# Kernel tuning notes

Measured on AMD Instinct MI355X. Metric: run time of the kernel, lower is better.

Reference implementation:

```python
import jax, jax.numpy as jnp
import numpy as np

B, C, H, W = 512, 1, 64, 64
T, L, Z = 32, 1024, 128
RS, WS = 12, 12


def _filterbank(g_x, g_y, logvar, logdelta, N):
    # g_x, g_y, logvar, logdelta: (B, 1)
    g_x = 0.5 * (W + 1) * (g_x + 1)
    g_y = 0.5 * (H + 1) * (g_y + 1)
    delta = (max(H, W) - 1) / (N - 1) * jnp.exp(logdelta)            # (B,1)
    offs = jnp.arange(1.0, 1.0 + N) - 0.5 * (N + 1)                  # (N,)
    mu_x = g_x + offs * delta                                        # (B,N)
    mu_y = g_y + offs * delta                                        # (B,N)
    inv2var = 0.5 / jnp.exp(logvar)[:, :, None]                      # (B,1,1)
    Fx = jnp.exp(-inv2var * (jnp.arange(1.0, 1.0 + W)[None, None, :] - mu_x[:, :, None]) ** 2)
    Fx = Fx / jnp.sum(Fx + 1e-8, axis=2, keepdims=True)              # (B,N,W)
    Fy = jnp.exp(-inv2var * (jnp.arange(1.0, 1.0 + H)[None, None, :] - mu_y[:, :, None]) ** 2)
    Fy = Fy / jnp.sum(Fy + 1e-8, axis=2, keepdims=True)              # (B,N,H)
    return Fx, Fy


def _lstm(x, h, c, Wih, Whh, bih, bhh):
    g = x @ Wih.T + bih + h @ Whh.T + bhh
    i, f, gg, o = jnp.split(g, 4, axis=1)
    c = jax.nn.sigmoid(f) * c + jax.nn.sigmoid(i) * jnp.tanh(gg)
    h = jax.nn.sigmoid(o) * jnp.tanh(c)
    return h, c


def setup_inputs() -> dict:
    key = jax.random.key(0)
    ks = jax.random.split(key, 9)
    s = 0.02
    return {
        'x': jax.random.uniform(ks[0], (B, C * H * W), jnp.float32),
        'enc_Wih': jax.random.normal(ks[1], (4 * L, 2 * RS * RS + L), jnp.float32) * s,
        'enc_Whh': jax.random.normal(ks[2], (4 * L, L), jnp.float32) * s,
        'enc_bih': jnp.zeros((4 * L,), jnp.float32),
        'enc_bhh': jnp.zeros((4 * L,), jnp.float32),
        'dec_Wih': jax.random.normal(ks[3], (4 * L, Z), jnp.float32) * s,
        'dec_Whh': jax.random.normal(ks[4], (4 * L, L), jnp.float32) * s,
        'dec_bih': jnp.zeros((4 * L,), jnp.float32),
        'dec_bhh': jnp.zeros((4 * L,), jnp.float32),
        'zW': jax.random.normal(ks[5], (2 * Z, L), jnp.float32) * s,
        'zb': jnp.zeros((2 * Z,), jnp.float32),
        'wW': jax.random.normal(ks[6], (WS * WS, L), jnp.float32) * s,
        'wb': jnp.zeros((WS * WS,), jnp.float32),
        'raW': jax.random.normal(ks[7], (5, L), jnp.float32) * s,
        'rab': jnp.zeros((5,), jnp.float32),
        'waW': jax.random.normal(ks[8], (5, L), jnp.float32) * s,
        'wab': jnp.zeros((5,), jnp.float32),
    }


def reference(x, enc_Wih, enc_Whh, enc_bih, enc_bhh, dec_Wih, dec_Whh, dec_bih, dec_bhh,
              zW, zb, wW, wb, raW, rab, waW, wab):
    def read(xf, x_hat, h_dec):
        a = h_dec @ raW.T + rab                                      # (B,5)
        g_x, g_y, logvar, logdelta, loggamma = jnp.split(a, 5, axis=1)
        Fx, Fy = _filterbank(g_x, g_y, logvar, logdelta, RS)
        nx = jnp.einsum('bnh,bhw,bmw->bnm', Fy, xf.reshape(-1, H, W), Fx)
        nxh = jnp.einsum('bnh,bhw,bmw->bnm', Fy, x_hat.reshape(-1, H, W), Fx)
        return jnp.exp(loggamma) * jnp.concatenate(
            [nx.reshape(nx.shape[0], -1), nxh.reshape(nxh.shape[0], -1)], axis=1)

    def write(h_dec):
        w = h_dec @ wW.T + wb                                        # (B, WS*WS)
        a = h_dec @ waW.T + wab
        g_x, g_y, logvar, logdelta, loggamma = jnp.split(a, 5, axis=1)
        Fx, Fy = _filterbank(g_x, g_y, logvar, logdelta, WS)
        wr = jnp.einsum('bnh,bnm,bmw->bhw', Fy, w.reshape(-1, WS, WS), Fx)
        return jnp.exp(-loggamma) * wr.reshape(wr.shape[0], -1)

    zkeys = jax.random.split(jax.random.key(42), T)

    def step(carry, key):
        c, h_enc, c_enc, h_dec, c_dec = carry
        x_hat = x - jax.nn.sigmoid(c)
        r = read(x, x_hat, h_dec)
        h_enc, c_enc = _lstm(jnp.concatenate([r, h_dec], axis=1), h_enc, c_enc,
                             enc_Wih, enc_Whh, enc_bih, enc_bhh)
        stats = h_enc @ zW.T + zb
        mu, logsig = jnp.split(stats, 2, axis=1)
        sig = jnp.exp(logsig)
        z = mu + sig * jax.random.normal(key, mu.shape, mu.dtype)
        h_dec, c_dec = _lstm(z, h_dec, c_dec, dec_Wih, dec_Whh, dec_bih, dec_bhh)
        c = c + write(h_dec)
        return (c, h_enc, c_enc, h_dec, c_dec), (mu, sig)

    c0 = jnp.zeros_like(x)
    h0 = jnp.zeros((x.shape[0], L), x.dtype)
    carry0 = (c0, h0, h0, h0, h0)
    (c, _, _, _, _), (mus, sigs) = jax.lax.scan(step, carry0, zkeys)
    # stack along last dim like torch.stack(mus, dim=-1): (B, Z, T)
    return c, jnp.moveaxis(mus, 0, -1), jnp.moveaxis(sigs, 0, -1)
```

## Files before the change

kernel.cpp:

```cpp
#include <hip/hip_runtime.h>
#include <cstdint>
#include <cstddef>

#define BB 512
#define TT 32
#define LL 1024
#define ZZ 128

typedef unsigned short ushort_t;
typedef __attribute__((ext_vector_type(8))) short s8v;
typedef __attribute__((ext_vector_type(4))) float f32x4;

__device__ __forceinline__ float sigf(float x) { return 1.0f / (1.0f + expf(-x)); }

__device__ __forceinline__ ushort_t f2bf(float f) {
  uint32_t u = __float_as_uint(f);
  uint32_t r = (u + 0x7FFFu + ((u >> 16) & 1u)) >> 16;
  return (ushort_t)r;
}
__device__ __forceinline__ float bf2f(ushort_t h) {
  return __uint_as_float(((uint32_t)h) << 16);
}
__device__ __forceinline__ void splitf(float v, ushort_t& hi, ushort_t& lo) {
  hi = f2bf(v);
  lo = f2bf(v - bf2f(hi));
}

__device__ __forceinline__ float jax_erfinv(float x) {
  float w = -log1pf(-x * x);
  float p;
  if (w < 5.0f) {
    w = w - 2.5f;
    p = 2.81022636e-08f;
    p = fmaf(p, w, 3.43273939e-07f);
    p = fmaf(p, w, -3.5233877e-06f);
    p = fmaf(p, w, -4.39150654e-06f);
    p = fmaf(p, w, 0.00021858087f);
    p = fmaf(p, w, -0.00125372503f);
    p = fmaf(p, w, -0.00417768164f);
    p = fmaf(p, w, 0.246640727f);
    p = fmaf(p, w, 1.50140941f);
  } else {
    w = sqrtf(w) - 3.0f;
    p = -0.000200214257f;
    p = fmaf(p, w, 0.000100950558f);
    p = fmaf(p, w, 0.00134934322f);
    p = fmaf(p, w, -0.00367342844f);
    p = fmaf(p, w, 0.00573950773f);
    p = fmaf(p, w, -0.0076224613f);
    p = fmaf(p, w, 0.00943887047f);
    p = fmaf(p, w, 1.00167406f);
    p = fmaf(p, w, 2.83297682f);
  }
  return p * x;
}

__device__ __forceinline__ void threefry(uint32_t k0, uint32_t k1,
                                         uint32_t x0, uint32_t x1,
                                         uint32_t& o0, uint32_t& o1) {
  uint32_t ks0 = k0, ks1 = k1, ks2 = k0 ^ k1 ^ 0x1BD11BDAu;
  x0 += ks0; x1 += ks1;
#define TF_ROT(x, d) (((x) << (d)) | ((x) >> (32 - (d))))
#define TF_RND(r) { x0 += x1; x1 = TF_ROT(x1, r); x1 ^= x0; }
  TF_RND(13) TF_RND(15) TF_RND(26) TF_RND(6)
  x0 += ks1; x1 += ks2 + 1u;
  TF_RND(17) TF_RND(29) TF_RND(16) TF_RND(24)
  x0 += ks2; x1 += ks0 + 2u;
  TF_RND(13) TF_RND(15) TF_RND(26) TF_RND(6)
  x0 += ks0; x1 += ks1 + 3u;
  TF_RND(17) TF_RND(29) TF_RND(16) TF_RND(24)
  x0 += ks1; x1 += ks2 + 4u;
  TF_RND(13) TF_RND(15) TF_RND(26) TF_RND(6)
  x0 += ks2; x1 += ks0 + 5u;
#undef TF_RND
#undef TF_ROT
  o0 = x0; o1 = x1;
}

__device__ __forceinline__ float bits_to_normal(uint32_t bits) {
  uint32_t fb = (bits >> 9) | 0x3f800000u;
  float f = __uint_as_float(fb) - 1.0f;
  const float lo = -0.99999994f;
  float u = fmaxf(lo, f * 2.0f + lo);
  return 1.41421356237f * jax_erfinv(u);
}

__global__ __launch_bounds__(256) void k_split(const float* __restrict__ src,
                                               ushort_t* __restrict__ hi,
                                               ushort_t* __restrict__ lo, int n) {
  int i = blockIdx.x * 256 + threadIdx.x;
  if (i >= n) return;
  ushort_t h, l;
  splitf(src[i], h, l);
  hi[i] = h; lo[i] = l;
}

__global__ void k_catbias(const float* __restrict__ wb, const float* __restrict__ wab,
                          float* __restrict__ cb) {
  int i = threadIdx.x;
  cb[i] = (i < 144) ? wb[i] : (i < 149 ? wab[i - 144] : 0.f);
}

struct Seg { const ushort_t* A; const ushort_t* W; int K; int lda; int ldw; };
struct SegList { Seg s[9]; int n; };

__device__ __forceinline__ void load_tiles(const Seg& sg, int bm, int bn, int N, int k0,
                                           int tid, s8v va[4], s8v vw[4]) {
#pragma unroll
  for (int i = 0; i < 4; ++i) {
    int cch = tid + 256 * i;
    int row = cch >> 3, col = cch & 7;
    va[i] = *(const s8v*)(sg.A + (size_t)(bm + row) * sg.lda + k0 + col * 8);
    int n = bn + row;
    if (n < N) vw[i] = *(const s8v*)(sg.W + (size_t)n * sg.ldw + k0 + col * 8);
    else       vw[i] = (s8v)(short)0;
  }
}

__global__ __launch_bounds__(256, 2) void mfma_gemm(
    float* __restrict__ C, unsigned zstride, int N, SegList segs, int ipz, int T) {
  __shared__ __align__(16) ushort_t As[128][72];
  __shared__ __align__(16) ushort_t Ws[128][72];
  const int z = blockIdx.z;
  C += (size_t)z * zstride;
  const int bm = blockIdx.y * 128, bn = blockIdx.x * 128;
  const int tid = threadIdx.x;
  const int w = tid >> 6, lane = tid & 63;
  const int wr = w >> 1, wc = w & 1;
  const int lr = lane & 15, lq = lane >> 4;
  f32x4 acc[4][4] = {};

  int it0 = z * ipz;
  int it1 = it0 + ipz; if (it1 > T) it1 = T;
  int iters = it1 - it0;
  if (iters > 0) {
    int si = 0, rem = it0;
    while (rem >= (segs.s[si].K >> 6)) { rem -= segs.s[si].K >> 6; ++si; }
    int k0 = rem << 6;
    s8v va[4], vw[4];
    load_tiles(segs.s[si], bm, bn, N, k0, tid, va, vw);
    for (int it = 0; it < iters; ++it) {
      __syncthreads();
#pragma unroll
      for (int i = 0; i < 4; ++i) {
        int cch = tid + 256 * i;
        *(s8v*)&As[cch >> 3][(cch & 7) * 8] = va[i];
        *(s8v*)&Ws[cch >> 3][(cch & 7) * 8] = vw[i];
      }
      __syncthreads();
      int nsi = si, nk0 = k0 + 64;
      if (nk0 >= segs.s[si].K) { nk0 = 0; ++nsi; }
      if (it + 1 < iters) load_tiles(segs.s[nsi], bm, bn, N, nk0, tid, va, vw);
#pragma unroll
      for (int ks = 0; ks < 2; ++ks) {
        s8v af[4], bf[4];
#pragma unroll
        for (int m = 0; m < 4; ++m)
          af[m] = *(const s8v*)&As[wr * 64 + m * 16 + lr][ks * 32 + lq * 8];
#pragma unroll
        for (int j = 0; j < 4; ++j)
          bf[j] = *(const s8v*)&Ws[wc * 64 + j * 16 + lr][ks * 32 + lq * 8];
#pragma unroll
        for (int m = 0; m < 4; ++m)
#pragma unroll
          for (int j = 0; j < 4; ++j)
            acc[m][j] = __builtin_amdgcn_mfma_f32_16x16x32_bf16(af[m], bf[j], acc[m][j], 0, 0, 0);
      }
      si = nsi; k0 = nk0;
    }
  }
#pragma unroll
  for (int j = 0; j < 4; ++j) {
    int col = bn + wc * 64 + j * 16 + lr;
    if (col < N) {
#pragma unroll
      for (int m = 0; m < 4; ++m)
#pragma unroll
        for (int q = 0; q < 4; ++q) {
          int rr = bm + wr * 64 + m * 16 + lq * 4 + q;
          C[(size_t)rr * N + col] = acc[m][j][q];
        }
    }
  }
}

__global__ __launch_bounds__(256) void k_fread(
    const float* __restrict__ x, const float* __restrict__ c,
    const float* __restrict__ rab,
    ushort_t* __restrict__ rH, ushort_t* __restrict__ rL) {
  int b = blockIdx.x;
  __shared__ float a_sh[5];
  __shared__ float fx[12][64], fy[12][64];
  __shared__ float srow[24];
  __shared__ float X[64][64];
  __shared__ float Xh[64][64];
  __shared__ float tmp[12][64], tmph[12][64];
  int tid = threadIdx.x;
  if (tid < 5) a_sh[tid] = rab[tid];
  for (int e = tid; e < 4096; e += 256) {
    float xv = x[(size_t)b * 4096 + e];
    float cv = c[(size_t)b * 4096 + e];
    X[e >> 6][e & 63] = xv;
    Xh[e >> 6][e & 63] = xv - sigf(cv);
  }
  __syncthreads();
  float gx = 32.5f * (a_sh[0] + 1.f);
  float gy = 32.5f * (a_sh[1] + 1.f);
  float i2v = 0.5f * expf(-a_sh[2]);
  float delta = (63.f / 11.f) * expf(a_sh[3]);
  float gam = expf(a_sh[4]);
  for (int e = tid; e < 768; e += 256) {
    int n = e >> 6, p = e & 63;
    float mu_x = gx + ((float)n - 5.5f) * delta;
    float mu_y = gy + ((float)n - 5.5f) * delta;
    float dx = (float)(p + 1) - mu_x;
    float dy = (float)(p + 1) - mu_y;
    fx[n][p] = expf(-i2v * dx * dx);
    fy[n][p] = expf(-i2v * dy * dy);
  }
  __syncthreads();
  if (tid < 24) {
    int n = tid % 12;
    float s = 0.f;
    if (tid < 12) { for (int p = 0; p < 64; ++p) s += fx[n][p]; }
    else          { for (int p = 0; p < 64; ++p) s += fy[n][p]; }
    srow[tid] = s + 6.4e-7f;
  }
  __syncthreads();
  for (int e = tid; e < 768; e += 256) {
    int n = e >> 6, p = e & 63;
    fx[n][p] /= srow[n];
    fy[n][p] /= srow[12 + n];
  }
  __syncthreads();
  for (int e = tid; e < 768; e += 256) {
    int n = e >> 6, w2 = e & 63;
    float s = 0.f, sh = 0.f;
    for (int hh = 0; hh < 64; ++hh) {
      float f = fy[n][hh];
      s  = fmaf(f, X[hh][w2], s);
      sh = fmaf(f, Xh[hh][w2], sh);
    }
    tmp[n][w2] = s; tmph[n][w2] = sh;
  }
  __syncthreads();
  if (tid < 144) {
    int n = tid / 12, m = tid % 12;
    float s = 0.f, sh = 0.f;
    for (int w2 = 0; w2 < 64; ++w2) {
      float f = fx[m][w2];
      s  = fmaf(tmp[n][w2], f, s);
      sh = fmaf(tmph[n][w2], f, sh);
    }
    float v0 = gam * s, v1 = gam * sh;
    size_t i0 = (size_t)b * 320 + n * 12 + m;
    size_t i1 = i0 + 144;
    ushort_t h0, l0, h1, l1;
    splitf(v0, h0, l0); splitf(v1, h1, l1);
    rH[i0] = h0; rL[i0] = l0;
    rH[i1] = h1; rL[i1] = l1;
  }
}

__global__ __launch_bounds__(256) void k_z(const float* __restrict__ parts,
                                           unsigned SZ, int nz,
                                           const float* __restrict__ zb,
                                           ushort_t* __restrict__ zH,
                                           ushort_t* __restrict__ zL,
                                           float* __restrict__ out_mu,
                                           float* __restrict__ out_sg, int t) {
  int i = blockIdx.x * 256 + threadIdx.x;
  int b = i >> 7, zi = i & 127;
  float mu = zb[zi], ls = zb[128 + zi];
  for (int z = 0; z < nz; ++z) {
    size_t base = (size_t)z * SZ + (size_t)b * 256;
    mu += parts[base + zi];
    ls += parts[base + 128 + zi];
  }
  uint32_t kA, kB, o0, o1;
  threefry(0u, 42u, 0u, (uint32_t)t, kA, kB);
  threefry(kA, kB, 0u, (uint32_t)i, o0, o1);
  float ep = bits_to_normal(o0 ^ o1);
  float sg = expf(ls);
  float zv = mu + sg * ep;
  ushort_t zh, zl;
  splitf(zv, zh, zl);
  zH[i] = zh; zL[i] = zl;
  out_mu[(size_t)b * 4096 + zi * 32 + t] = mu;
  out_sg[(size_t)b * 4096 + zi * 32 + t] = sg;
}

__global__ __launch_bounds__(256) void k_fwr(
    float* __restrict__ c, const float* __restrict__ x,
    const float* __restrict__ parts, unsigned WZ, int nz,
    const float* __restrict__ cb, const float* __restrict__ rab,
    ushort_t* __restrict__ rH, ushort_t* __restrict__ rL, int last) {
  int b = blockIdx.x;
  __shared__ float red[160];
  __shared__ float a_sh[5];
  __shared__ float fx[12][64], fy[12][64];
  __shared__ float srow[24];
  __shared__ float tmp[12][64], tmph[12][64];
  __shared__ float X[64][64];
  __shared__ float Xh[64][64];
  int tid = threadIdx.x;
  if (tid < 154) {
    float s = cb[tid];
    for (int z = 0; z < nz; ++z) s += parts[(size_t)z * WZ + (size_t)b * 176 + tid];
    red[tid] = s;
  }
  __syncthreads();
  {
    float gx = 32.5f * (red[144] + 1.f);
    float gy = 32.5f * (red[145] + 1.f);
    float i2v = 0.5f * expf(-red[146]);
    float delta = (63.f / 11.f) * expf(red[147]);
    for (int e = tid; e < 768; e += 256) {
      int n = e >> 6, p = e & 63;
      float mu_x = gx + ((float)n - 5.5f) * delta;
      float mu_y = gy + ((float)n - 5.5f) * delta;
      float dx = (float)(p + 1) - mu_x;
      float dy = (float)(p + 1) - mu_y;
      fx[n][p] = expf(-i2v * dx * dx);
      fy[n][p] = expf(-i2v * dy * dy);
    }
  }
  __syncthreads();
  if (tid < 24) {
    int n = tid % 12;
    float s = 0.f;
    if (tid < 12) { for (int p = 0; p < 64; ++p) s += fx[n][p]; }
    else          { for (int p = 0; p < 64; ++p) s += fy[n][p]; }
    srow[tid] = s + 6.4e-7f;
  }
  __syncthreads();
  for (int e = tid; e < 768; e += 256) {
    int n = e >> 6, p = e & 63;
    fx[n][p] /= srow[n];
    fy[n][p] /= srow[12 + n];
  }
  __syncthreads();
  for (int e = tid; e < 768; e += 256) {
    int n = e >> 6, w2 = e & 63;
    float s = 0.f;
#pragma unroll
    for (int m = 0; m < 12; ++m) s = fmaf(red[n * 12 + m], fx[m][w2], s);
    tmp[n][w2] = s;
  }
  __syncthreads();
  {
    float gam = expf(-red[148]);
    for (int e = tid; e < 4096; e += 256) {
      int hh = e >> 6, w2 = e & 63;
      float s = 0.f;
#pragma unroll
      for (int n = 0; n < 12; ++n) s = fmaf(fy[n][hh], tmp[n][w2], s);
      float cv = c[(size_t)b * 4096 + e] + gam * s;
      c[(size_t)b * 4096 + e] = cv;
      float xv = x[(size_t)b * 4096 + e];
      X[hh][w2] = xv;
      Xh[hh][w2] = xv - sigf(cv);
    }
  }
  if (last) return;
  if (tid < 5) a_sh[tid] = red[149 + tid] + rab[tid];
  __syncthreads();
  {
    float gx = 32.5f * (a_sh[0] + 1.f);
    float gy = 32.5f * (a_sh[1] + 1.f);
    float i2v = 0.5f * expf(-a_sh[2]);
    float delta = (63.f / 11.f) * expf(a_sh[3]);
    for (int e = tid; e < 768; e += 256) {
      int n = e >> 6, p = e & 63;
      float mu_x = gx + ((float)n - 5.5f) * delta;
      float mu_y = gy + ((float)n - 5.5f) * delta;
      float dx = (float)(p + 1) - mu_x;
      float dy = (float)(p + 1) - mu_y;
      fx[n][p] = expf(-i2v * dx * dx);
      fy[n][p] = expf(-i2v * dy * dy);
    }
  }
  __syncthreads();
  if (tid < 24) {
    int n = tid % 12;
    float s = 0.f;
    if (tid < 12) { for (int p = 0; p < 64; ++p) s += fx[n][p]; }
    else          { for (int p = 0; p < 64; ++p) s += fy[n][p]; }
    srow[tid] = s + 6.4e-7f;
  }
  __syncthreads();
  for (int e = tid; e < 768; e += 256) {
    int n = e >> 6, p = e & 63;
    fx[n][p] /= srow[n];
    fy[n][p] /= srow[12 + n];
  }
  __syncthreads();
  for (int e = tid; e < 768; e += 256) {
    int n = e >> 6, w2 = e & 63;
    float s = 0.f, sh = 0.f;
    for (int hh = 0; hh < 64; ++hh) {
      float f = fy[n][hh];
      s  = fmaf(f, X[hh][w2], s);
      sh = fmaf(f, Xh[hh][w2], sh);
    }
    tmp[n][w2] = s; tmph[n][w2] = sh;
  }
  __syncthreads();
  if (tid < 144) {
    float gam = expf(a_sh[4]);
    int n = tid / 12, m = tid % 12;
    float s = 0.f, sh = 0.f;
    for (int w2 = 0; w2 < 64; ++w2) {
      float f = fx[m][w2];
      s  = fmaf(tmp[n][w2], f, s);
      sh = fmaf(tmph[n][w2], f, sh);
    }
    float v0 = gam * s, v1 = gam * sh;
    size_t i0 = (size_t)b * 320 + n * 12 + m;
    size_t i1 = i0 + 144;
    ushort_t h0, l0, h1, l1;
    splitf(v0, h0, l0); splitf(v1, h1, l1);
    rH[i0] = h0; rL[i0] = l0;
    rH[i1] = h1; rL[i1] = l1;
  }
}

typedef unsigned short us4 __attribute__((ext_vector_type(4)));
__global__ __launch_bounds__(256) void k_lstm(const float* __restrict__ g,
                                              unsigned GZ, int nz,
                                              const float* __restrict__ bih,
                                              const float* __restrict__ bhh,
                                              float* __restrict__ cst,
                                              ushort_t* __restrict__ hH,
                                              ushort_t* __restrict__ hL) {
  int q = blockIdx.x * 256 + threadIdx.x;
  int b = q >> 8, uq = q & 255;
  size_t base = (size_t)b * 1024;
  float4 ig = *(const float4*)&bih[uq * 4];
  float4 fg = *(const float4*)&bih[1024 + uq * 4];
  float4 gg = *(const float4*)&bih[2048 + uq * 4];
  float4 og = *(const float4*)&bih[3072 + uq * 4];
  {
    float4 t0 = *(const float4*)&bhh[uq * 4];
    float4 t1 = *(const float4*)&bhh[1024 + uq * 4];
    float4 t2 = *(const float4*)&bhh[2048 + uq * 4];
    float4 t3 = *(const float4*)&bhh[3072 + uq * 4];
    ig.x += t0.x; ig.y += t0.y; ig.z += t0.z; ig.w += t0.w;
    fg.x += t1.x; fg.y += t1.y; fg.z += t1.z; fg.w += t1.w;
    gg.x += t2.x; gg.y += t2.y; gg.z += t2.z; gg.w += t2.w;
    og.x += t3.x; og.y += t3.y; og.z += t3.z; og.w += t3.w;
  }
  for (int z = 0; z < nz; ++z) {
    const float* gz = g + (size_t)z * GZ + base * 4;
    float4 t0 = *(const float4*)&gz[uq * 4];
    float4 t1 = *(const float4*)&gz[1024 + uq * 4];
    float4 t2 = *(const float4*)&gz[2048 + uq * 4];
    float4 t3 = *(const float4*)&gz[3072 + uq * 4];
    ig.x += t0.x; ig.y += t0.y; ig.z += t0.z; ig.w += t0.w;
    fg.x += t1.x; fg.y += t1.y; fg.z += t1.z; fg.w += t1.w;
    gg.x += t2.x; gg.y += t2.y; gg.z += t2.z; gg.w += t2.w;
    og.x += t3.x; og.y += t3.y; og.z += t3.z; og.w += t3.w;
  }
  float4 cv = *(const float4*)&cst[(size_t)q * 4];
  float cva[4] = {cv.x, cv.y, cv.z, cv.w};
  float iga[4] = {ig.x, ig.y, ig.z, ig.w};
  float fga[4] = {fg.x, fg.y, fg.z, fg.w};
  float gga[4] = {gg.x, gg.y, gg.z, gg.w};
  float oga[4] = {og.x, og.y, og.z, og.w};
  us4 hhv, hlv;
  float cvo[4];
#pragma unroll
  for (int j = 0; j < 4; ++j) {
    float cnew = sigf(fga[j]) * cva[j] + sigf(iga[j]) * tanhf(gga[j]);
    cvo[j] = cnew;
    float hv = sigf(oga[j]) * tanhf(cnew);
    ushort_t hh, hl;
    splitf(hv, hh, hl);
    hhv[j] = hh; hlv[j] = hl;
  }
  *(float4*)&cst[(size_t)q * 4] = make_float4(cvo[0], cvo[1], cvo[2], cvo[3]);
  *(us4*)&hH[(size_t)q * 4] = hhv;
  *(us4*)&hL[(size_t)q * 4] = hlv;
}

extern "C" void kernel_launch(void* const* d_in, const int* in_sizes, int n_in,
                              void* d_out, int out_size, void* d_ws, size_t ws_size,
                              hipStream_t stream) {
  const float* x       = (const float*)d_in[0];
  const float* enc_Wih = (const float*)d_in[1];
  const float* enc_Whh = (const float*)d_in[2];
  const float* enc_bih = (const float*)d_in[3];
  const float* enc_bhh = (const float*)d_in[4];
  const float* dec_Wih = (const float*)d_in[5];
  const float* dec_Whh = (const float*)d_in[6];
  const float* dec_bih = (const float*)d_in[7];
  const float* dec_bhh = (const float*)d_in[8];
  const float* zW  = (const float*)d_in[9];
  const float* zb  = (const float*)d_in[10];
  const float* wW  = (const float*)d_in[11];
  const float* wb  = (const float*)d_in[12];
  const float* raW = (const float*)d_in[13];
  const float* rab = (const float*)d_in[14];
  const float* waW = (const float*)d_in[15];
  const float* wab = (const float*)d_in[16];

  float* out = (float*)d_out;
  float* c      = out;
  float* out_mu = out + 2097152;
  float* out_sg = out + 4194304;

  int NZ = 4;
  size_t need = 0;
  for (int pass = 0; pass < 2; ++pass) {
    size_t off = 0;
    auto sz = [&](size_t bytes) { off = (off + bytes + 255) & ~(size_t)255; };
    sz(2097152); sz(2097152);
    sz(1048576); sz(1048576); sz(1048576); sz(1048576);
    sz(327680); sz(327680);
    sz(360448); sz(360448);
    sz(131072); sz(131072);
    sz((size_t)NZ * 8388608);
    sz(704);
    sz(10747904); sz(10747904);
    sz(8388608); sz(8388608);
    sz(1048576); sz(1048576);
    sz(8388608); sz(8388608);
    sz(524288); sz(524288);
    need = off;
    if (pass == 0 && ws_size < need) NZ = 2; else break;
  }

  char* base = (char*)d_ws;
  size_t off = 0;
  auto alloc = [&](size_t bytes) -> char* {
    char* p = base + off;
    off = (off + bytes + 255) & ~(size_t)255;
    return p;
  };
  float* c_enc = (float*)alloc(2097152);
  float* c_dec = (float*)alloc(2097152);
  ushort_t* hdH = (ushort_t*)alloc(1048576);
  ushort_t* hdL = (ushort_t*)alloc(1048576);
  ushort_t* heH = (ushort_t*)alloc(1048576);
  ushort_t* heL = (ushort_t*)alloc(1048576);
  ushort_t* rH  = (ushort_t*)alloc(327680);
  ushort_t* rL  = (ushort_t*)alloc(327680);
  ushort_t* cWH = (ushort_t*)alloc(360448);
  ushort_t* cWL = (ushort_t*)alloc(360448);
  size_t zero_bytes = off;
  ushort_t* zH = (ushort_t*)alloc(131072);
  ushort_t* zL = (ushort_t*)alloc(131072);
  float* gbuf  = (float*)alloc((size_t)NZ * 8388608);
  float* cb    = (float*)alloc(704);
  ushort_t* eWihH = (ushort_t*)alloc(10747904);
  ushort_t* eWihL = (ushort_t*)alloc(10747904);
  ushort_t* eWhhH = (ushort_t*)alloc(8388608);
  ushort_t* eWhhL = (ushort_t*)alloc(8388608);
  ushort_t* dWihH = (ushort_t*)alloc(1048576);
  ushort_t* dWihL = (ushort_t*)alloc(1048576);
  ushort_t* dWhhH = (ushort_t*)alloc(8388608);
  ushort_t* dWhhL = (ushort_t*)alloc(8388608);
  ushort_t* zWH   = (ushort_t*)alloc(524288);
  ushort_t* zWL   = (ushort_t*)alloc(524288);

  hipMemsetAsync(c, 0, (size_t)2097152 * sizeof(float), stream);
  hipMemsetAsync(base, 0, zero_bytes, stream);

  k_split<<<(5373952 + 255) / 256, 256, 0, stream>>>(enc_Wih, eWihH, eWihL, 5373952);
  k_split<<<(4194304 + 255) / 256, 256, 0, stream>>>(enc_Whh, eWhhH, eWhhL, 4194304);
  k_split<<<(524288 + 255) / 256, 256, 0, stream>>>(dec_Wih, dWihH, dWihL, 524288);
  k_split<<<(4194304 + 255) / 256, 256, 0, stream>>>(dec_Whh, dWhhH, dWhhL, 4194304);
  k_split<<<(262144 + 255) / 256, 256, 0, stream>>>(zW, zWH, zWL, 262144);
  k_split<<<(147456 + 255) / 256, 256, 0, stream>>>(wW, cWH, cWL, 147456);
  k_split<<<(5120 + 255) / 256, 256, 0, stream>>>(waW, cWH + 147456, cWL + 147456, 5120);
  k_split<<<(5120 + 255) / 256, 256, 0, stream>>>(raW, cWH + 152576, cWL + 152576, 5120);
  k_catbias<<<1, 176, 0, stream>>>(wb, wab, cb);

  SegList encS;
  encS.n = 9;
  encS.s[0] = {rH,  eWihH,       320,  320, 1312};
  encS.s[1] = {rL,  eWihH,       320,  320, 1312};
  encS.s[2] = {rH,  eWihL,       320,  320, 1312};
  encS.s[3] = {hdH, eWihH + 288, 1024, 1024, 1312};
  encS.s[4] = {hdL, eWihH + 288, 1024, 1024, 1312};
  encS.s[5] = {hdH, eWihL + 288, 1024, 1024, 1312};
  encS.s[6] = {heH, eWhhH,       1024, 1024, 1024};
  encS.s[7] = {heL, eWhhH,       1024, 1024, 1024};
  encS.s[8] = {heH, eWhhL,       1024, 1024, 1024};
  SegList decS;
  decS.n = 6;
  decS.s[0] = {zH,  dWihH, 128,  128, 128};
  decS.s[1] = {zL,  dWihH, 128,  128, 128};
  decS.s[2] = {zH,  dWihL, 128,  128, 128};
  decS.s[3] = {hdH, dWhhH, 1024, 1024, 1024};
  decS.s[4] = {hdL, dWhhH, 1024, 1024, 1024};
  decS.s[5] = {hdH, dWhhL, 1024, 1024, 1024};
  SegList staS;
  staS.n = 3;
  staS.s[0] = {heH, zWH, 1024, 1024, 1024};
  staS.s[1] = {heL, zWH, 1024, 1024, 1024};
  staS.s[2] = {heH, zWL, 1024, 1024, 1024};
  SegList wvS;
  wvS.n = 3;
  wvS.s[0] = {hdH, cWH, 1024, 1024, 1024};
  wvS.s[1] = {hdL, cWH, 1024, 1024, 1024};
  wvS.s[2] = {hdH, cWL, 1024, 1024, 1024};

  const unsigned GZ = 2097152;
  const unsigned SZ = 131072;
  const unsigned WZ = 90112;
  const int ipz_e = (111 + NZ - 1) / NZ;
  const int ipz_d = (54 + NZ - 1) / NZ;

  k_fread<<<512, 256, 0, stream>>>(x, c, rab, rH, rL);
  for (int t = 0; t < TT; ++t) {
    mfma_gemm<<<dim3(32, 4, NZ), 256, 0, stream>>>(gbuf, GZ, 4096, encS, ipz_e, 111);
    k_lstm<<<512, 256, 0, stream>>>(gbuf, GZ, NZ, enc_bih, enc_bhh, c_enc, heH, heL);
    mfma_gemm<<<dim3(2, 4, 8), 256, 0, stream>>>(gbuf, SZ, 256, staS, 6, 48);
    k_z<<<256, 256, 0, stream>>>(gbuf, SZ, 8, zb, zH, zL, out_mu, out_sg, t);
    mfma_gemm<<<dim3(32, 4, NZ), 256, 0, stream>>>(gbuf, GZ, 4096, decS, ipz_d, 54);
    k_lstm<<<512, 256, 0, stream>>>(gbuf, GZ, NZ, dec_bih, dec_bhh, c_dec, hdH, hdL);
    mfma_gemm<<<dim3(2, 4, 8), 256, 0, stream>>>(gbuf, WZ, 176, wvS, 6, 48);
    k_fwr<<<512, 256, 0, stream>>>(c, x, gbuf, WZ, 8, cb, rab, rH, rL, t == TT - 1);
  }
}
```

Measured before the change: 3.918 ms.

## Stream GEMM tiles directly into double-buffered swizzled LDS via global_load_lds

Replaces the register-staged global-to-LDS tile copy in the MFMA GEMM with direct global_load_lds transfers into a double-buffered, XOR-swizzled shared-memory layout. The next tile's load is issued before computing on the current one, with explicit vmcnt/lgkmcnt waits and barriers. Because the N bounds check is removed, the write-vector weight buffer and its output are padded to 256 columns, which k_fwr now indexes with a 256 stride. This aims to cut VGPR staging, LDS bank conflicts and load latency, but it doubles LDS use and depends on the hand-written waitcnt ordering being correct.

Measured after the change: 3.763 ms, median of 2. 3.9% less time.

```diff
diff --git a/kernel.cpp b/kernel.cpp
--- a/kernel.cpp
+++ b/kernel.cpp
@@ -101,26 +101,34 @@
   cb[i] = (i < 144) ? wb[i] : (i < 149 ? wab[i - 144] : 0.f);
 }
 
+__device__ __forceinline__ void gload16(const ushort_t* g, ushort_t* l) {
+  __builtin_amdgcn_global_load_lds(
+      (const __attribute__((address_space(1))) unsigned int*)g,
+      (__attribute__((address_space(3))) unsigned int*)l, 16, 0, 0);
+}
+
 struct Seg { const ushort_t* A; const ushort_t* W; int K; int lda; int ldw; };
 struct SegList { Seg s[9]; int n; };
 
-__device__ __forceinline__ void load_tiles(const Seg& sg, int bm, int bn, int N, int k0,
-                                           int tid, s8v va[4], s8v vw[4]) {
+__device__ __forceinline__ void issue_tile(const Seg& sg, int bm, int bn, int k0,
+                                           int tid, ushort_t* Ab, ushort_t* Wb) {
+  const int w = tid >> 6, lane = tid & 63;
+  const int sub = lane >> 3;
+  const int colE = (((lane & 7) ^ sub) << 3);
 #pragma unroll
   for (int i = 0; i < 4; ++i) {
-    int cch = tid + 256 * i;
-    int row = cch >> 3, col = cch & 7;
-    va[i] = *(const s8v*)(sg.A + (size_t)(bm + row) * sg.lda + k0 + col * 8);
-    int n = bn + row;
-    if (n < N) vw[i] = *(const s8v*)(sg.W + (size_t)n * sg.ldw + k0 + col * 8);
-    else       vw[i] = (s8v)(short)0;
+    int row = w * 32 + i * 8 + sub;
+    ushort_t* ldst = Ab + w * 2048 + i * 512;
+    gload16(sg.A + (size_t)(bm + row) * sg.lda + k0 + colE, ldst);
+    ushort_t* ldstw = Wb + w * 2048 + i * 512;
+    gload16(sg.W + (size_t)(bn + row) * sg.ldw + k0 + colE, ldstw);
   }
 }
 
 __global__ __launch_bounds__(256, 2) void mfma_gemm(
     float* __restrict__ C, unsigned zstride, int N, SegList segs, int ipz, int T) {
-  __shared__ __align__(16) ushort_t As[128][72];
-  __shared__ __align__(16) ushort_t Ws[128][72];
+  __shared__ __align__(16) ushort_t As[2][128][64];
+  __shared__ __align__(16) ushort_t Ws[2][128][64];
   const int z = blockIdx.z;
   C += (size_t)z * zstride;
   const int bm = blockIdx.y * 128, bn = blockIdx.x * 128;
@@ -128,6 +136,7 @@
   const int w = tid >> 6, lane = tid & 63;
   const int wr = w >> 1, wc = w & 1;
   const int lr = lane & 15, lq = lane >> 4;
+  const int swz = lr & 7;
   f32x4 acc[4][4] = {};
 
   int it0 = z * ipz;
@@ -137,36 +146,37 @@
     int si = 0, rem = it0;
     while (rem >= (segs.s[si].K >> 6)) { rem -= segs.s[si].K >> 6; ++si; }
     int k0 = rem << 6;
-    s8v va[4], vw[4];
-    load_tiles(segs.s[si], bm, bn, N, k0, tid, va, vw);
+    issue_tile(segs.s[si], bm, bn, k0, tid, &As[0][0][0], &Ws[0][0][0]);
+    int cur = 0;
     for (int it = 0; it < iters; ++it) {
-      __syncthreads();
-#pragma unroll
-      for (int i = 0; i < 4; ++i) {
-        int cch = tid + 256 * i;
-        *(s8v*)&As[cch >> 3][(cch & 7) * 8] = va[i];
-        *(s8v*)&Ws[cch >> 3][(cch & 7) * 8] = vw[i];
-      }
-      __syncthreads();
       int nsi = si, nk0 = k0 + 64;
       if (nk0 >= segs.s[si].K) { nk0 = 0; ++nsi; }
-      if (it + 1 < iters) load_tiles(segs.s[nsi], bm, bn, N, nk0, tid, va, vw);
+      const bool more = (it + 1 < iters);
+      asm volatile("s_waitcnt lgkmcnt(0)" ::: "memory");
+      __builtin_amdgcn_s_barrier();
+      if (more) {
+        issue_tile(segs.s[nsi], bm, bn, nk0, tid, &As[cur ^ 1][0][0], &Ws[cur ^ 1][0][0]);
+        asm volatile("s_waitcnt vmcnt(8)" ::: "memory");
+      } else {
+        asm volatile("s_waitcnt vmcnt(0)" ::: "memory");
+      }
+      __builtin_amdgcn_s_barrier();
 #pragma unroll
       for (int ks = 0; ks < 2; ++ks) {
         s8v af[4], bf[4];
 #pragma unroll
-        for (int m = 0; m < 4; ++m)
-          af[m] = *(const s8v*)&As[wr * 64 + m * 16 + lr][ks * 32 + lq * 8];
-#pragma unroll
-        for (int j = 0; j < 4; ++j)
-          bf[j] = *(const s8v*)&Ws[wc * 64 + j * 16 + lr][ks * 32 + lq * 8];
+        for (int m = 0; m < 4; ++m) {
+          int chunk = ((ks * 4 + lq) ^ swz) * 8;
+          af[m] = *(const s8v*)&As[cur][wr * 64 + m * 16 + lr][chunk];
+          bf[m] = *(const s8v*)&Ws[cur][wc * 64 + m * 16 + lr][chunk];
+        }
 #pragma unroll
         for (int m = 0; m < 4; ++m)
 #pragma unroll
           for (int j = 0; j < 4; ++j)
             acc[m][j] = __builtin_amdgcn_mfma_f32_16x16x32_bf16(af[m], bf[j], acc[m][j], 0, 0, 0);
       }
-      si = nsi; k0 = nk0;
+      cur ^= 1; si = nsi; k0 = nk0;
     }
   }
 #pragma unroll
@@ -306,7 +316,7 @@
   int tid = threadIdx.x;
   if (tid < 154) {
     float s = cb[tid];
-    for (int z = 0; z < nz; ++z) s += parts[(size_t)z * WZ + (size_t)b * 176 + tid];
+    for (int z = 0; z < nz; ++z) s += parts[(size_t)z * WZ + (size_t)b * 256 + tid];
     red[tid] = s;
   }
   __syncthreads();
@@ -517,7 +527,7 @@
     sz(2097152); sz(2097152);
     sz(1048576); sz(1048576); sz(1048576); sz(1048576);
     sz(327680); sz(327680);
-    sz(360448); sz(360448);
+    sz(524288); sz(524288);
     sz(131072); sz(131072);
     sz((size_t)NZ * 8388608);
     sz(704);
@@ -545,8 +555,8 @@
   ushort_t* heL = (ushort_t*)alloc(1048576);
   ushort_t* rH  = (ushort_t*)alloc(327680);
   ushort_t* rL  = (ushort_t*)alloc(327680);
-  ushort_t* cWH = (ushort_t*)alloc(360448);
-  ushort_t* cWL = (ushort_t*)alloc(360448);
+  ushort_t* cWH = (ushort_t*)alloc(524288);
+  ushort_t* cWL = (ushort_t*)alloc(524288);
   size_t zero_bytes = off;
   ushort_t* zH = (ushort_t*)alloc(131072);
   ushort_t* zL = (ushort_t*)alloc(131072);
@@ -608,7 +618,7 @@
 
   const unsigned GZ = 2097152;
   const unsigned SZ = 131072;
-  const unsigned WZ = 90112;
+  const unsigned WZ = 131072;
   const int ipz_e = (111 + NZ - 1) / NZ;
   const int ipz_d = (54 + NZ - 1) / NZ;
 
@@ -620,7 +630,7 @@
     k_z<<<256, 256, 0, stream>>>(gbuf, SZ, 8, zb, zH, zL, out_mu, out_sg, t);
     mfma_gemm<<<dim3(32, 4, NZ), 256, 0, stream>>>(gbuf, GZ, 4096, decS, ipz_d, 54);
     k_lstm<<<512, 256, 0, stream>>>(gbuf, GZ, NZ, dec_bih, dec_bhh, c_dec, hdH, hdL);
-    mfma_gemm<<<dim3(2, 4, 8), 256, 0, stream>>>(gbuf, WZ, 176, wvS, 6, 48);
+    mfma_gemm<<<dim3(2, 4, 8), 256, 0, stream>>>(gbuf, WZ, 256, wvS, 6, 48);
     k_fwr<<<512, 256, 0, stream>>>(c, x, gbuf, WZ, 8, cb, rab, rH, rL, t == TT - 1);
   }
 }
```
